# Kernel tuning notes

Measured on AMD Instinct MI355X. Metric: run time of the kernel, lower is better.

## Reference

```python
import jax, jax.numpy as jnp
import numpy as np

NUM_NODES = 1_000_000
IN_F, HID_F, OUT_F = 128, 128, 128
N0, N1, T = 16384, 4096, 16


def _safediv(a, b):
    return a / jnp.where(b == 0, jnp.ones_like(b), b)


def _conv(h, nodeset, nb_nodes, nb_w, Qw, Qb, Ww, Wb):
    # gather self + neighbor embeddings (irregular access)
    h_self = h[nodeset]                                   # [n, in]
    h_nb = h[nb_nodes]                                    # [n, T, in]
    q = jax.nn.leaky_relu(jnp.einsum('nti,hi->nth', h_nb, Qw) + Qb)
    agg = _safediv((nb_w[:, :, None] * q).sum(1), nb_w.sum(1, keepdims=True))  # [n, hid]
    h_cat = jnp.concatenate([h_self, agg], axis=1)        # [n, in+hid]
    h_new = jax.nn.leaky_relu(h_cat @ Ww.T + Wb)          # [n, out]
    nrm = jnp.linalg.norm(h_new, axis=1, keepdims=True)
    return _safediv(h_new, nrm)


def setup_inputs() -> dict:
    key = jax.random.key(0)
    ks = jax.random.split(key, 16)
    xav = lambda k, o, i: jax.random.uniform(k, (o, i), jnp.float32, -1.0, 1.0) * jnp.sqrt(6.0 / (o + i)) * jnp.sqrt(2.0)
    return {
        'h': jax.random.normal(ks[0], (NUM_NODES, IN_F), jnp.float32),
        'Qw0': xav(ks[1], HID_F, IN_F), 'Qb0': jnp.zeros((HID_F,), jnp.float32),
        'Ww0': xav(ks[2], HID_F, IN_F + HID_F), 'Wb0': jnp.zeros((HID_F,), jnp.float32),
        'Qw1': xav(ks[3], OUT_F, HID_F), 'Qb1': jnp.zeros((OUT_F,), jnp.float32),
        'Ww1': xav(ks[4], OUT_F, HID_F + OUT_F), 'Wb1': jnp.zeros((OUT_F,), jnp.float32),
        'nodeset0': jax.random.randint(ks[5], (N0,), 0, NUM_NODES, jnp.int32),
        'nb_nodes0': jax.random.randint(ks[6], (N0, T), 0, NUM_NODES, jnp.int32),
        'nb_weights0': jax.random.uniform(ks[7], (N0, T), jnp.float32),
        'nodeset1': jax.random.randint(ks[8], (N1,), 0, NUM_NODES, jnp.int32),
        'nb_nodes1': jax.random.randint(ks[9], (N1, T), 0, NUM_NODES, jnp.int32),
        'nb_weights1': jax.random.uniform(ks[10], (N1, T), jnp.float32),
    }


def reference(h, Qw0, Qb0, Ww0, Wb0, Qw1, Qb1, Ww1, Wb1,
              nodeset0, nb_nodes0, nb_weights0,
              nodeset1, nb_nodes1, nb_weights1):
    # layer 0: conv then scatter back into embedding table
    new0 = _conv(h, nodeset0, nb_nodes0, nb_weights0, Qw0, Qb0, Ww0, Wb0)
    h = h.at[nodeset0].set(new0)
    # layer 1
    new1 = _conv(h, nodeset1, nb_nodes1, nb_weights1, Qw1, Qb1, Ww1, Wb1)
    h = h.at[nodeset1].set(new1)
    return h[nodeset1]  # [N1, OUT_F]
```

## Files before the change

### kernel.cpp

```cpp
#include <hip/hip_runtime.h>
#include <hip/hip_bf16.h>
#include <math.h>

#define NN 1000000
#define F 128
#define N0 16384
#define N1 4096
#define HS0 65536
#define HS1 16384

typedef __attribute__((ext_vector_type(8))) short bf16x8;
typedef __attribute__((ext_vector_type(4))) float f32x4;

__device__ inline unsigned short f2b(float f) {
    union { float f; unsigned u; } v; v.f = f;
    unsigned r = v.u + 0x7FFFu + ((v.u >> 16) & 1u);
    return (unsigned short)(r >> 16);
}

__device__ inline bf16x8 pack8(float4 a, float4 b) {
    union { __hip_bfloat162 h2[4]; bf16x8 v; } u;
    u.h2[0] = __float22bfloat162_rn(make_float2(a.x, a.y));
    u.h2[1] = __float22bfloat162_rn(make_float2(a.z, a.w));
    u.h2[2] = __float22bfloat162_rn(make_float2(b.x, b.y));
    u.h2[3] = __float22bfloat162_rn(make_float2(b.z, b.w));
    return u.v;
}

__device__ inline uint2 pack4(float4 a) {
    union { __hip_bfloat162 h2[2]; uint2 v; } u;
    u.h2[0] = __float22bfloat162_rn(make_float2(a.x, a.y));
    u.h2[1] = __float22bfloat162_rn(make_float2(a.z, a.w));
    return u.v;
}

__device__ inline int kperm(int p) {
    int kk = p >> 5, kg = (p >> 3) & 3, e = p & 7;
    return kk * 32 + kg * 4 + (e < 4 ? e : e + 12);
}


__device__ inline void hins(unsigned* __restrict__ keys, unsigned* __restrict__ vals,
                            unsigned mask, unsigned g, unsigned pos1) {
    unsigned s = (g * 2654435761u) & mask;
    while (true) {
        unsigned prev = atomicCAS(&keys[s], 0xFFFFFFFFu, g);
        if (prev == 0xFFFFFFFFu || prev == g) { atomicMax(&vals[s], pos1); return; }
        s = (s + 1) & mask;
    }
}

__device__ inline int hfind(const unsigned* __restrict__ keys,
                            const unsigned* __restrict__ vals,
                            unsigned mask, unsigned g) {
    unsigned s = (g * 2654435761u) & mask;
    while (true) {
        unsigned k = keys[s];
        if (k == g) return (int)vals[s] - 1;
        if (k == 0xFFFFFFFFu) return -1;
        s = (s + 1) & mask;
    }
}


__global__ void k_pre(unsigned* __restrict__ k0, unsigned* __restrict__ v0,
                      unsigned* __restrict__ k1, unsigned* __restrict__ v1,
                      const float* __restrict__ Qw0, const float* __restrict__ Qw1,
                      const float* __restrict__ Ww0, const float* __restrict__ Ww1,
                      unsigned short* __restrict__ Qw0b, unsigned short* __restrict__ Qw1b,
                      unsigned short* __restrict__ Ww0b, unsigned short* __restrict__ Ww1b) {
    int i = blockIdx.x * blockDim.x + threadIdx.x;
    int nt = gridDim.x * blockDim.x;
    for (int j = i; j < HS0; j += nt) { k0[j] = 0xFFFFFFFFu; v0[j] = 0u; }
    for (int j = i; j < HS1; j += nt) { k1[j] = 0xFFFFFFFFu; v1[j] = 0u; }
    for (int j = i; j < 128 * 128; j += nt) {
        int r = j >> 7, p = j & 127;
        int src = (r << 7) + kperm(p);
        Qw0b[j] = f2b(Qw0[src]); Qw1b[j] = f2b(Qw1[src]);
    }
    for (int j = i; j < 128 * 256; j += nt) {
        int r = j >> 8, p = j & 255;
        int src = (r << 8) + (p < 128 ? kperm(p) : p);
        Ww0b[j] = f2b(Ww0[src]); Ww1b[j] = f2b(Ww1[src]);
    }
}


__global__ __launch_bounds__(512, 4) void k_layer(
    const float* __restrict__ h, const unsigned short* __restrict__ newprevb,
    const unsigned* __restrict__ lk, const unsigned* __restrict__ lv, unsigned lmask,
    const int* __restrict__ nodeset, const int* __restrict__ nb,
    const float* __restrict__ nbw,
    const unsigned short* __restrict__ Qwb, const float* __restrict__ Qb,
    const unsigned short* __restrict__ Wwb, const float* __restrict__ Wb,
    float* __restrict__ outf, unsigned short* __restrict__ outb,
    const int* __restrict__ ins0, unsigned* __restrict__ ik0, unsigned* __restrict__ iv0,
    const int* __restrict__ ins1, unsigned* __restrict__ ik1, unsigned* __restrict__ iv1)
{
    __shared__ unsigned short lQ[128 * 128];
    __shared__ unsigned short lA[16 * 256];
    __shared__ float sred[8][16];
    const int tid = threadIdx.x;
    const int wid = tid >> 6, lane = tid & 63;
    const int row = lane & 15, kg = lane >> 4;
    const long mbase = (long)blockIdx.x * 16;

    if (ik0) {
        int base = blockIdx.x * 16;
        if (tid < 16) {
            int i = base + tid;
            if (i < N0) hins(ik0, iv0, HS0 - 1, (unsigned)ins0[i], (unsigned)(i + 1));
        } else if (tid < 32) {
            int i = base + tid - 16;
            if (i < N1) hins(ik1, iv1, HS1 - 1, (unsigned)ins1[i], (unsigned)(i + 1));
        }
    }

    const int sr = tid >> 4, sq = tid & 15;
    const bool sact = tid < 256;
    bool sredir = false;
    float4 sv0, sv1;
    uint4 sb;
    if (sact) {
        int gs = nodeset[mbase + sr];
        int p = lk ? hfind(lk, lv, lmask, (unsigned)gs) : -1;
        if (p >= 0) {
            sredir = true;
            sb = *(const uint4*)(newprevb + (size_t)p * F + sq * 8);
        } else {
            const float4* s = (const float4*)(h + (size_t)gs * F);
            sv0 = s[sq]; sv1 = s[sq + 16];
        }
    }

    const long nodebase = mbase + wid * 2;
    int g0 = nb[nodebase * 16 + row];
    int g1 = nb[(nodebase + 1) * 16 + row];
    int p0 = lk ? hfind(lk, lv, lmask, (unsigned)g0) : -1;
    int p1 = lk ? hfind(lk, lv, lmask, (unsigned)g1) : -1;
    bf16x8 Ab[2][4];
    float4 av[2][8];
    if (p0 >= 0) {
        const bf16x8* s = (const bf16x8*)(newprevb + (size_t)p0 * F);
#pragma unroll
        for (int kk = 0; kk < 4; ++kk) Ab[0][kk] = s[kk * 4 + kg];
    } else {
        const float4* s4 = (const float4*)(h + (size_t)g0 * F);
#pragma unroll
        for (int c = 0; c < 8; ++c) av[0][c] = s4[c * 4 + kg];
    }
    if (p1 >= 0) {
        const bf16x8* s = (const bf16x8*)(newprevb + (size_t)p1 * F);
#pragma unroll
        for (int kk = 0; kk < 4; ++kk) Ab[1][kk] = s[kk * 4 + kg];
    } else {
        const float4* s4 = (const float4*)(h + (size_t)g1 * F);
#pragma unroll
        for (int c = 0; c < 8; ++c) av[1][c] = s4[c * 4 + kg];
    }

    for (int c = tid; c < 2048; c += 512) {
        int j = c >> 4;
        uint4 v = ((const uint4*)Qwb)[c];
        *(uint4*)((char*)lQ + ((c << 4) ^ ((j & 7) << 4))) = v;
    }

    float w[2][4];
#pragma unroll
    for (int nn = 0; nn < 2; ++nn)
#pragma unroll
        for (int r = 0; r < 4; ++r) w[nn][r] = nbw[(nodebase + nn) * 16 + kg * 4 + r];

    if (p0 < 0) {
#pragma unroll
        for (int kk = 0; kk < 4; ++kk) Ab[0][kk] = pack8(av[0][2 * kk], av[0][2 * kk + 1]);
    }
    if (p1 < 0) {
#pragma unroll
        for (int kk = 0; kk < 4; ++kk) Ab[1][kk] = pack8(av[1][2 * kk], av[1][2 * kk + 1]);
    }

    if (sact) {
        int swz = (sr & 7) << 4;
        if (sredir) {
            int b0 = sr * 512 + sq * 16;
            *(uint4*)((char*)lA + (b0 ^ swz)) = sb;
        } else {
            int pp = ((sq >> 3) << 5) + ((sq & 3) << 3) + ((sq & 4) ? 4 : 0);
            int b1 = sr * 512 + pp * 2;
            *(uint2*)((char*)lA + (b1 ^ swz)) = pack4(sv0);
            *(uint2*)((char*)lA + ((b1 + 128) ^ swz)) = pack4(sv1);
        }
    }
    __syncthreads();

    float inv[2];
#pragma unroll
    for (int nn = 0; nn < 2; ++nn) {
        float ws = w[nn][0] + w[nn][1] + w[nn][2] + w[nn][3];
        ws += __shfl_xor(ws, 16);
        ws += __shfl_xor(ws, 32);
        inv[nn] = (ws == 0.f) ? 1.f : 1.f / ws;
    }

#pragma unroll 1
    for (int half = 0; half < 2; ++half) {
        f32x4 acc[2][4];
#pragma unroll
        for (int nn = 0; nn < 2; ++nn)
#pragma unroll
            for (int jt = 0; jt < 4; ++jt)
                acc[nn][jt] = (f32x4){0.f, 0.f, 0.f, 0.f};

#pragma unroll
        for (int kk = 0; kk < 4; ++kk) {
            bf16x8 Bf[4];
#pragma unroll
            for (int jt = 0; jt < 4; ++jt) {
                int j = (half * 4 + jt) * 16 + row;
                int byte = ((j << 8) + (kk << 6) + (kg << 4)) ^ ((j & 7) << 4);
                Bf[jt] = *(bf16x8*)((char*)lQ + byte);
            }
#pragma unroll
            for (int jt = 0; jt < 4; ++jt) {
                acc[0][jt] = __builtin_amdgcn_mfma_f32_16x16x32_bf16(Ab[0][kk], Bf[jt], acc[0][jt], 0, 0, 0);
                acc[1][jt] = __builtin_amdgcn_mfma_f32_16x16x32_bf16(Ab[1][kk], Bf[jt], acc[1][jt], 0, 0, 0);
            }
        }

#pragma unroll
        for (int nn = 0; nn < 2; ++nn) {
            int nl = wid * 2 + nn;
#pragma unroll
            for (int jt = 0; jt < 4; ++jt) {
                int jtg = half * 4 + jt;
                float qb = Qb[jtg * 16 + row];
                float t = 0.f;
#pragma unroll
                for (int r = 0; r < 4; ++r) {
                    float v = acc[nn][jt][r] + qb;
                    v = v > 0.f ? v : 0.01f * v;
                    t = fmaf(w[nn][r], v, t);
                }
                t += __shfl_xor(t, 16);
                t += __shfl_xor(t, 32);
                if (lane < 16) {
                    int byte = (nl * 512 + 256 + jtg * 32 + lane * 2) ^ ((nl & 7) << 4);
                    *(unsigned short*)((char*)lA + byte) = f2b(t * inv[nn]);
                }
            }
        }
    }
    __syncthreads();

    const int j = wid * 16 + row;
    f32x4 dacc = (f32x4){0.f, 0.f, 0.f, 0.f};
#pragma unroll
    for (int kk = 0; kk < 8; ++kk) {
        bf16x8 a = *(bf16x8*)((char*)lA + ((row * 512 + kk * 64 + kg * 16) ^ ((row & 7) << 4)));
        bf16x8 b = ((const bf16x8*)(Wwb + (size_t)j * 256))[kk * 4 + kg];
        dacc = __builtin_amdgcn_mfma_f32_16x16x32_bf16(a, b, dacc, 0, 0, 0);
    }

    float wb = Wb[j];
    float ss[4];
#pragma unroll
    for (int r = 0; r < 4; ++r) {
        float v = dacc[r] + wb;
        v = v > 0.f ? v : 0.01f * v;
        dacc[r] = v;
        ss[r] = v * v;
    }
#pragma unroll
    for (int r = 0; r < 4; ++r) {
        ss[r] += __shfl_xor(ss[r], 1);
        ss[r] += __shfl_xor(ss[r], 2);
        ss[r] += __shfl_xor(ss[r], 4);
        ss[r] += __shfl_xor(ss[r], 8);
    }
    if (row == 0) {
#pragma unroll
        for (int r = 0; r < 4; ++r) sred[wid][kg * 4 + r] = ss[r];
    }
    __syncthreads();
    float invn[4];
#pragma unroll
    for (int r = 0; r < 4; ++r) {
        float s = 0.f;
#pragma unroll
        for (int w8 = 0; w8 < 8; ++w8) s += sred[w8][kg * 4 + r];
        float n = sqrtf(s);
        invn[r] = (n == 0.f) ? 1.f : 1.f / n;
    }
    if (outf) {
#pragma unroll
        for (int r = 0; r < 4; ++r)
            outf[(size_t)(mbase + kg * 4 + r) * F + j] = dacc[r] * invn[r];
    } else {
        int pj = ((j >> 5) << 5) + (((j & 15) >> 2) << 3) + ((j & 16) ? 4 : 0) + (j & 3);
#pragma unroll
        for (int r = 0; r < 4; ++r)
            outb[(size_t)(mbase + kg * 4 + r) * F + pj] = f2b(dacc[r] * invn[r]);
    }
}


__global__ void k_fix(const unsigned* __restrict__ k1, const unsigned* __restrict__ v1,
                      const int* __restrict__ ns1, float* __restrict__ out, int n) {
    int i = blockIdx.x * blockDim.x + threadIdx.x;
    if (i < n) {
        int p = hfind(k1, v1, HS1 - 1, (unsigned)ns1[i]);
        if (p != i) {
            float4* o = (float4*)out;
#pragma unroll
            for (int c = 0; c < 32; ++c) o[(size_t)i * 32 + c] = o[(size_t)p * 32 + c];
        }
    }
}


extern "C" void kernel_launch(void* const* d_in, const int* in_sizes, int n_in,
                              void* d_out, int out_size, void* d_ws, size_t ws_size,
                              hipStream_t stream) {
    const float* h    = (const float*)d_in[0];
    const float* Qw0  = (const float*)d_in[1];
    const float* Qb0  = (const float*)d_in[2];
    const float* Ww0  = (const float*)d_in[3];
    const float* Wb0  = (const float*)d_in[4];
    const float* Qw1  = (const float*)d_in[5];
    const float* Qb1  = (const float*)d_in[6];
    const float* Ww1  = (const float*)d_in[7];
    const float* Wb1  = (const float*)d_in[8];
    const int*   ns0  = (const int*)d_in[9];
    const int*   nb0  = (const int*)d_in[10];
    const float* nbw0 = (const float*)d_in[11];
    const int*   ns1  = (const int*)d_in[12];
    const int*   nb1  = (const int*)d_in[13];
    const float* nbw1 = (const float*)d_in[14];

    unsigned* hk0 = (unsigned*)d_ws;
    unsigned* hv0 = hk0 + HS0;
    unsigned* hk1 = hv0 + HS0;
    unsigned* hv1 = hk1 + HS1;
    unsigned short* new0b = (unsigned short*)(hv1 + HS1);
    unsigned short* Qw0b = new0b + (size_t)N0 * F;
    unsigned short* Qw1b = Qw0b + 128 * 128;
    unsigned short* Ww0b = Qw1b + 128 * 128;
    unsigned short* Ww1b = Ww0b + 128 * 256;

    k_pre<<<128, 256, 0, stream>>>(hk0, hv0, hk1, hv1,
                                   Qw0, Qw1, Ww0, Ww1, Qw0b, Qw1b, Ww0b, Ww1b);

    k_layer<<<N0 / 16, 512, 0, stream>>>(h, nullptr, nullptr, nullptr, 0u,
                                         ns0, nb0, nbw0, Qw0b, Qb0, Ww0b, Wb0,
                                         nullptr, new0b,
                                         ns0, hk0, hv0, ns1, hk1, hv1);

    k_layer<<<N1 / 16, 512, 0, stream>>>(h, new0b, hk0, hv0, HS0 - 1,
                                         ns1, nb1, nbw1, Qw1b, Qb1, Ww1b, Wb1,
                                         (float*)d_out, nullptr,
                                         nullptr, nullptr, nullptr, nullptr, nullptr, nullptr);

    k_fix<<<(N1 + 255) / 256, 256, 0, stream>>>(hk1, hv1, ns1, (float*)d_out, N1);
}
```

Before: 79.55 us.

## Halve nodes per block to one node per wave and double the grid

```diff
diff --git a/kernel.cpp b/kernel.cpp
--- a/kernel.cpp
+++ b/kernel.cpp
@@ -86,7 +86,7 @@
 }
 
 
-__global__ __launch_bounds__(512, 4) void k_layer(
+__global__ __launch_bounds__(512, 5) void k_layer(
     const float* __restrict__ h, const unsigned short* __restrict__ newprevb,
     const unsigned* __restrict__ lk, const unsigned* __restrict__ lv, unsigned lmask,
     const int* __restrict__ nodeset, const int* __restrict__ nb,
@@ -103,21 +103,20 @@
     const int tid = threadIdx.x;
     const int wid = tid >> 6, lane = tid & 63;
     const int row = lane & 15, kg = lane >> 4;
-    const long mbase = (long)blockIdx.x * 16;
+    const long mbase = (long)blockIdx.x * 8;
 
     if (ik0) {
-        int base = blockIdx.x * 16;
-        if (tid < 16) {
-            int i = base + tid;
-            if (i < N0) hins(ik0, iv0, HS0 - 1, (unsigned)ins0[i], (unsigned)(i + 1));
-        } else if (tid < 32) {
-            int i = base + tid - 16;
-            if (i < N1) hins(ik1, iv1, HS1 - 1, (unsigned)ins1[i], (unsigned)(i + 1));
+        if (tid < 8) {
+            int i = (int)mbase + tid;
+            hins(ik0, iv0, HS0 - 1, (unsigned)ins0[i], (unsigned)(i + 1));
+        } else if (tid < 16 && blockIdx.x < 512) {
+            int i = (int)mbase + tid - 8;
+            hins(ik1, iv1, HS1 - 1, (unsigned)ins1[i], (unsigned)(i + 1));
         }
     }
 
     const int sr = tid >> 4, sq = tid & 15;
-    const bool sact = tid < 256;
+    const bool sact = tid < 128;
     bool sredir = false;
     float4 sv0, sv1;
     uint4 sb;
@@ -133,30 +132,19 @@
         }
     }
 
-    const long nodebase = mbase + wid * 2;
-    int g0 = nb[nodebase * 16 + row];
-    int g1 = nb[(nodebase + 1) * 16 + row];
-    int p0 = lk ? hfind(lk, lv, lmask, (unsigned)g0) : -1;
-    int p1 = lk ? hfind(lk, lv, lmask, (unsigned)g1) : -1;
-    bf16x8 Ab[2][4];
-    float4 av[2][8];
-    if (p0 >= 0) {
-        const bf16x8* s = (const bf16x8*)(newprevb + (size_t)p0 * F);
-#pragma unroll
-        for (int kk = 0; kk < 4; ++kk) Ab[0][kk] = s[kk * 4 + kg];
+    const long node = mbase + wid;
+    int g = nb[node * 16 + row];
+    int p = lk ? hfind(lk, lv, lmask, (unsigned)g) : -1;
+    bf16x8 Ab[4];
+    float4 av[8];
+    if (p >= 0) {
+        const bf16x8* s = (const bf16x8*)(newprevb + (size_t)p * F);
+#pragma unroll
+        for (int kk = 0; kk < 4; ++kk) Ab[kk] = s[kk * 4 + kg];
     } else {
-        const float4* s4 = (const float4*)(h + (size_t)g0 * F);
-#pragma unroll
-        for (int c = 0; c < 8; ++c) av[0][c] = s4[c * 4 + kg];
-    }
-    if (p1 >= 0) {
-        const bf16x8* s = (const bf16x8*)(newprevb + (size_t)p1 * F);
-#pragma unroll
-        for (int kk = 0; kk < 4; ++kk) Ab[1][kk] = s[kk * 4 + kg];
-    } else {
-        const float4* s4 = (const float4*)(h + (size_t)g1 * F);
-#pragma unroll
-        for (int c = 0; c < 8; ++c) av[1][c] = s4[c * 4 + kg];
+        const float4* s4 = (const float4*)(h + (size_t)g * F);
+#pragma unroll
+        for (int c = 0; c < 8; ++c) av[c] = s4[c * 4 + kg];
     }
 
     for (int c = tid; c < 2048; c += 512) {
@@ -165,19 +153,15 @@
         *(uint4*)((char*)lQ + ((c << 4) ^ ((j & 7) << 4))) = v;
     }
 
-    float w[2][4];
-#pragma unroll
-    for (int nn = 0; nn < 2; ++nn)
-#pragma unroll
-        for (int r = 0; r < 4; ++r) w[nn][r] = nbw[(nodebase + nn) * 16 + kg * 4 + r];
-
-    if (p0 < 0) {
-#pragma unroll
-        for (int kk = 0; kk < 4; ++kk) Ab[0][kk] = pack8(av[0][2 * kk], av[0][2 * kk + 1]);
-    }
-    if (p1 < 0) {
-#pragma unroll
-        for (int kk = 0; kk < 4; ++kk) Ab[1][kk] = pack8(av[1][2 * kk], av[1][2 * kk + 1]);
+    ((uint2*)((char*)lA + 4096))[tid] = make_uint2(0u, 0u);
+
+    float w[4];
+#pragma unroll
+    for (int r = 0; r < 4; ++r) w[r] = nbw[node * 16 + kg * 4 + r];
+
+    if (p < 0) {
+#pragma unroll
+        for (int kk = 0; kk < 4; ++kk) Ab[kk] = pack8(av[2 * kk], av[2 * kk + 1]);
     }
 
     if (sact) {
@@ -194,23 +178,16 @@
     }
     __syncthreads();
 
-    float inv[2];
-#pragma unroll
-    for (int nn = 0; nn < 2; ++nn) {
-        float ws = w[nn][0] + w[nn][1] + w[nn][2] + w[nn][3];
-        ws += __shfl_xor(ws, 16);
-        ws += __shfl_xor(ws, 32);
-        inv[nn] = (ws == 0.f) ? 1.f : 1.f / ws;
-    }
+    float ws = w[0] + w[1] + w[2] + w[3];
+    ws += __shfl_xor(ws, 16);
+    ws += __shfl_xor(ws, 32);
+    float inv = (ws == 0.f) ? 1.f : 1.f / ws;
 
 #pragma unroll 1
     for (int half = 0; half < 2; ++half) {
-        f32x4 acc[2][4];
-#pragma unroll
-        for (int nn = 0; nn < 2; ++nn)
-#pragma unroll
-            for (int jt = 0; jt < 4; ++jt)
-                acc[nn][jt] = (f32x4){0.f, 0.f, 0.f, 0.f};
+        f32x4 acc[4];
+#pragma unroll
+        for (int jt = 0; jt < 4; ++jt) acc[jt] = (f32x4){0.f, 0.f, 0.f, 0.f};
 
 #pragma unroll
         for (int kk = 0; kk < 4; ++kk) {
@@ -222,32 +199,26 @@
                 Bf[jt] = *(bf16x8*)((char*)lQ + byte);
             }
 #pragma unroll
-            for (int jt = 0; jt < 4; ++jt) {
-                acc[0][jt] = __builtin_amdgcn_mfma_f32_16x16x32_bf16(Ab[0][kk], Bf[jt], acc[0][jt], 0, 0, 0);
-                acc[1][jt] = __builtin_amdgcn_mfma_f32_16x16x32_bf16(Ab[1][kk], Bf[jt], acc[1][jt], 0, 0, 0);
+            for (int jt = 0; jt < 4; ++jt)
+                acc[jt] = __builtin_amdgcn_mfma_f32_16x16x32_bf16(Ab[kk], Bf[jt], acc[jt], 0, 0, 0);
+        }
+
+#pragma unroll
+        for (int jt = 0; jt < 4; ++jt) {
+            int jtg = half * 4 + jt;
+            float qb = Qb[jtg * 16 + row];
+            float t = 0.f;
+#pragma unroll
+            for (int r = 0; r < 4; ++r) {
+                float v = acc[jt][r] + qb;
+                v = v > 0.f ? v : 0.01f * v;
+                t = fmaf(w[r], v, t);
             }
-        }
-
-#pragma unroll
-        for (int nn = 0; nn < 2; ++nn) {
-            int nl = wid * 2 + nn;
-#pragma unroll
-            for (int jt = 0; jt < 4; ++jt) {
-                int jtg = half * 4 + jt;
-                float qb = Qb[jtg * 16 + row];
-                float t = 0.f;
-#pragma unroll
-                for (int r = 0; r < 4; ++r) {
-                    float v = acc[nn][jt][r] + qb;
-                    v = v > 0.f ? v : 0.01f * v;
-                    t = fmaf(w[nn][r], v, t);
-                }
-                t += __shfl_xor(t, 16);
-                t += __shfl_xor(t, 32);
-                if (lane < 16) {
-                    int byte = (nl * 512 + 256 + jtg * 32 + lane * 2) ^ ((nl & 7) << 4);
-                    *(unsigned short*)((char*)lA + byte) = f2b(t * inv[nn]);
-                }
+            t += __shfl_xor(t, 16);
+            t += __shfl_xor(t, 32);
+            if (lane < 16) {
+                int byte = (wid * 512 + 256 + jtg * 32 + lane * 2) ^ ((wid & 7) << 4);
+                *(unsigned short*)((char*)lA + byte) = f2b(t * inv);
             }
         }
     }
@@ -283,24 +254,26 @@
         for (int r = 0; r < 4; ++r) sred[wid][kg * 4 + r] = ss[r];
     }
     __syncthreads();
-    float invn[4];
-#pragma unroll
-    for (int r = 0; r < 4; ++r) {
-        float s = 0.f;
-#pragma unroll
-        for (int w8 = 0; w8 < 8; ++w8) s += sred[w8][kg * 4 + r];
-        float n = sqrtf(s);
-        invn[r] = (n == 0.f) ? 1.f : 1.f / n;
-    }
-    if (outf) {
-#pragma unroll
-        for (int r = 0; r < 4; ++r)
-            outf[(size_t)(mbase + kg * 4 + r) * F + j] = dacc[r] * invn[r];
-    } else {
-        int pj = ((j >> 5) << 5) + (((j & 15) >> 2) << 3) + ((j & 16) ? 4 : 0) + (j & 3);
-#pragma unroll
-        for (int r = 0; r < 4; ++r)
-            outb[(size_t)(mbase + kg * 4 + r) * F + pj] = f2b(dacc[r] * invn[r]);
+    if (kg < 2) {
+        float invn[4];
+#pragma unroll
+        for (int r = 0; r < 4; ++r) {
+            float s = 0.f;
+#pragma unroll
+            for (int w8 = 0; w8 < 8; ++w8) s += sred[w8][kg * 4 + r];
+            float n = sqrtf(s);
+            invn[r] = (n == 0.f) ? 1.f : 1.f / n;
+        }
+        if (outf) {
+#pragma unroll
+            for (int r = 0; r < 4; ++r)
+                outf[(size_t)(mbase + kg * 4 + r) * F + j] = dacc[r] * invn[r];
+        } else {
+            int pj = ((j >> 5) << 5) + (((j & 15) >> 2) << 3) + ((j & 16) ? 4 : 0) + (j & 3);
+#pragma unroll
+            for (int r = 0; r < 4; ++r)
+                outb[(size_t)(mbase + kg * 4 + r) * F + pj] = f2b(dacc[r] * invn[r]);
+        }
     }
 }
 
@@ -351,15 +324,15 @@
     k_pre<<<128, 256, 0, stream>>>(hk0, hv0, hk1, hv1,
                                    Qw0, Qw1, Ww0, Ww1, Qw0b, Qw1b, Ww0b, Ww1b);
 
-    k_layer<<<N0 / 16, 512, 0, stream>>>(h, nullptr, nullptr, nullptr, 0u,
-                                         ns0, nb0, nbw0, Qw0b, Qb0, Ww0b, Wb0,
-                                         nullptr, new0b,
-                                         ns0, hk0, hv0, ns1, hk1, hv1);
-
-    k_layer<<<N1 / 16, 512, 0, stream>>>(h, new0b, hk0, hv0, HS0 - 1,
-                                         ns1, nb1, nbw1, Qw1b, Qb1, Ww1b, Wb1,
-                                         (float*)d_out, nullptr,
-                                         nullptr, nullptr, nullptr, nullptr, nullptr, nullptr);
+    k_layer<<<N0 / 8, 512, 0, stream>>>(h, nullptr, nullptr, nullptr, 0u,
+                                        ns0, nb0, nbw0, Qw0b, Qb0, Ww0b, Wb0,
+                                        nullptr, new0b,
+                                        ns0, hk0, hv0, ns1, hk1, hv1);
+
+    k_layer<<<N1 / 8, 512, 0, stream>>>(h, new0b, hk0, hv0, HS0 - 1,
+                                        ns1, nb1, nbw1, Qw1b, Qb1, Ww1b, Wb1,
+                                        (float*)d_out, nullptr,
+                                        nullptr, nullptr, nullptr, nullptr, nullptr, nullptr);
 
     k_fix<<<(N1 + 255) / 256, 256, 0, stream>>>(hk1, hv1, ns1, (float*)d_out, N1);
 }
```

Result: slower. 87.86 us (+10.4%).
